# Kernel tuning notes

Hardware: AMD Instinct MI355X
Metric: run time of the kernel (lower is better)

Reference implementation:

```python
import jax, jax.numpy as jnp
import numpy as np

NUM_ITERATIONS = 3
NUM_SLOTS = 8
SLOT_SIZE = 256
MLP_HIDDEN = 512
EPSILON = 1e-8
LN_EPS = 1e-5


def _ln(x, w, b):
    m = jnp.mean(x, axis=-1, keepdims=True)
    v = jnp.var(x, axis=-1, keepdims=True)
    return (x - m) * jax.lax.rsqrt(v + LN_EPS) * w + b


def _gru_cell(x, h, w_ih, w_hh, b_ih, b_hh):
    # torch.nn.GRUCell semantics; gates ordered [r, z, n]
    gi = x @ w_ih.T + b_ih
    gh = h @ w_hh.T + b_hh
    ir, iz, inn = jnp.split(gi, 3, axis=-1)
    hr, hz, hn = jnp.split(gh, 3, axis=-1)
    r = jax.nn.sigmoid(ir + hr)
    z = jax.nn.sigmoid(iz + hz)
    n = jnp.tanh(inn + r * hn)
    return (1.0 - z) * n + z * h


def setup_inputs() -> dict:
    key = jax.random.key(0)
    ks = jax.random.split(key, 12)
    D, H = SLOT_SIZE, MLP_HIDDEN
    s = 0.02
    return {
        "inputs": jax.random.normal(ks[0], (64, 4096, D), dtype=jnp.float32),
        "noise": jax.random.normal(ks[1], (64, NUM_SLOTS, D), dtype=jnp.float32),
        "ln_in_w": jnp.ones((D,), jnp.float32), "ln_in_b": jnp.zeros((D,), jnp.float32),
        "ln_slots_w": jnp.ones((D,), jnp.float32), "ln_slots_b": jnp.zeros((D,), jnp.float32),
        "ln_mlp_w": jnp.ones((D,), jnp.float32), "ln_mlp_b": jnp.zeros((D,), jnp.float32),
        "slots_mu": jax.random.normal(ks[2], (1, 1, D), jnp.float32) * s,
        "slots_log_sigma": jnp.zeros((1, 1, D), jnp.float32),
        "Wq": jax.random.normal(ks[3], (D, D), jnp.float32) * s,
        "Wk": jax.random.normal(ks[4], (D, D), jnp.float32) * s,
        "Wv": jax.random.normal(ks[5], (D, D), jnp.float32) * s,
        "gru_w_ih": jax.random.normal(ks[6], (3 * D, D), jnp.float32) * s,
        "gru_w_hh": jax.random.normal(ks[7], (3 * D, D), jnp.float32) * s,
        "gru_b_ih": jnp.zeros((3 * D,), jnp.float32),
        "gru_b_hh": jnp.zeros((3 * D,), jnp.float32),
        "mlp_w1": jax.random.normal(ks[8], (H, D), jnp.float32) * s,
        "mlp_b1": jnp.zeros((H,), jnp.float32),
        "mlp_w2": jax.random.normal(ks[9], (D, H), jnp.float32) * s,
        "mlp_b2": jnp.zeros((D,), jnp.float32),
    }


def reference(inputs, noise, ln_in_w, ln_in_b, ln_slots_w, ln_slots_b, ln_mlp_w, ln_mlp_b,
              slots_mu, slots_log_sigma, Wq, Wk, Wv,
              gru_w_ih, gru_w_hh, gru_b_ih, gru_b_hh,
              mlp_w1, mlp_b1, mlp_w2, mlp_b2):
    B, N, D = inputs.shape
    S = NUM_SLOTS
    x = _ln(inputs, ln_in_w, ln_in_b)            # [B,N,D]
    k = x @ Wk.T                                  # [B,N,D]
    v = x @ Wv.T                                  # [B,N,D]
    slots = slots_mu + jnp.exp(slots_log_sigma) * noise   # [B,S,D]
    scale = D ** (-0.5)
    for _ in range(NUM_ITERATIONS):
        slots_prev = slots
        s_n = _ln(slots, ln_slots_w, ln_slots_b)
        q = (s_n @ Wq.T) * scale                  # [B,S,D]
        attn_logits = jnp.einsum('bnd,bsd->bns', k, q)
        attn = jax.nn.softmax(attn_logits, axis=-1) + EPSILON
        attn = attn / jnp.sum(attn, axis=-2, keepdims=True)   # renorm over inputs
        updates = jnp.einsum('bns,bnd->bsd', attn, v)          # [B,S,D]
        slots = _gru_cell(updates.reshape(-1, D), slots_prev.reshape(-1, D),
                          gru_w_ih, gru_w_hh, gru_b_ih, gru_b_hh).reshape(B, S, D)
        h = jax.nn.relu(_ln(slots, ln_mlp_w, ln_mlp_b) @ mlp_w1.T + mlp_b1)
        slots = slots + (h @ mlp_w2.T + mlp_b2)
    return slots
```

## Files before the change

kernel.cpp:

```cpp
#include <hip/hip_runtime.h>

#define CB 64
#define CN 4096
#define CD 256
#define CS 8
#define CH 512

typedef __bf16 bf16_t;
typedef bf16_t bf16x8 __attribute__((ext_vector_type(8)));
typedef float f32x4 __attribute__((ext_vector_type(4)));

__device__ __forceinline__ unsigned short f2bf(float f){
  unsigned int u = __builtin_bit_cast(unsigned int, f);
  u += 0x7FFFu + ((u >> 16) & 1u);
  return (unsigned short)(u >> 16);
}

__device__ __forceinline__ f32x4 mfma16(bf16x8 a, bf16x8 b, f32x4 c){
  return __builtin_amdgcn_mfma_f32_16x16x32_bf16(a, b, c, 0, 0, 0);
}

__device__ __forceinline__ void gl_lds16(const void* g, void* l){
  __builtin_amdgcn_global_load_lds(
      (const __attribute__((address_space(1))) unsigned int*)g,
      (__attribute__((address_space(3))) unsigned int*)l, 16, 0, 0);
}

__global__ __launch_bounds__(256) void k_ln(const float* __restrict__ in,
    const float* __restrict__ gw, const float* __restrict__ gb,
    unsigned short* __restrict__ x){
  int blk = blockIdx.x;
  int b = blk >> 6, nt = blk & 63;
  int wv = threadIdx.x >> 6, l = threadIdx.x & 63;
  const float* base = in + ((size_t)b*CN + (size_t)nt*64) * CD;
  unsigned short* xb = x + ((size_t)b*CN + (size_t)nt*64) * CD;
  float4 w4 = *(const float4*)(gw + 4*l);
  float4 b4 = *(const float4*)(gb + 4*l);
  for(int i = 0; i < 16; i++){
    int r = wv*16 + i;
    float4 v = *(const float4*)(base + (size_t)r*CD + 4*l);
    float s1 = v.x + v.y + v.z + v.w;
    float s2 = v.x*v.x + v.y*v.y + v.z*v.z + v.w*v.w;
    #pragma unroll
    for(int m = 1; m < 64; m <<= 1){ s1 += __shfl_xor(s1, m); s2 += __shfl_xor(s2, m); }
    float mean = s1 * (1.0f/CD);
    float var  = fmaxf(s2 * (1.0f/CD) - mean*mean, 0.0f);
    float rstd = rsqrtf(var + 1e-5f);
    float y0 = (v.x - mean)*rstd*w4.x + b4.x;
    float y1 = (v.y - mean)*rstd*w4.y + b4.y;
    float y2 = (v.z - mean)*rstd*w4.z + b4.z;
    float y3 = (v.w - mean)*rstd*w4.w + b4.w;
    uint2 p;
    p.x = (unsigned)f2bf(y0) | ((unsigned)f2bf(y1) << 16);
    p.y = (unsigned)f2bf(y2) | ((unsigned)f2bf(y3) << 16);
    *(uint2*)(xb + (size_t)r*CD + 4*l) = p;
  }
}

__global__ __launch_bounds__(256) void k_setup(
    const float* __restrict__ Wq, const float* __restrict__ Wk,
    const float* __restrict__ wih, const float* __restrict__ Wv,
    const float* __restrict__ whh, const float* __restrict__ w1,
    const float* __restrict__ w2, const float* __restrict__ noise,
    const float* __restrict__ mu, const float* __restrict__ lsig,
    unsigned short* __restrict__ M1T, unsigned short* __restrict__ Mih_bf,
    unsigned short* __restrict__ Whh_bf, unsigned short* __restrict__ w1_bf,
    unsigned short* __restrict__ w2_bf, float* __restrict__ slots){
  int bid = blockIdx.x, tid = threadIdx.x;
  if(bid < 256){
    int ep = bid, e = tid;
    float acc = 0.0f;
    for(int d = 0; d < 256; d++) acc = fmaf(Wq[(size_t)d*256 + e], Wk[(size_t)d*256 + ep], acc);
    M1T[(size_t)ep*256 + e] = f2bf(acc * 0.0625f);
  } else if(bid < 1024){
    int j = bid - 256, e = tid;
    float acc = 0.0f;
    for(int d = 0; d < 256; d++) acc = fmaf(wih[(size_t)j*256 + d], Wv[(size_t)d*256 + e], acc);
    Mih_bf[(size_t)j*256 + e] = f2bf(acc);
  } else if(bid < 1792){
    int idx = (bid - 1024)*256 + tid;
    Whh_bf[idx] = f2bf(whh[idx]);
  } else if(bid < 2304){
    int idx = (bid - 1792)*256 + tid;
    w1_bf[idx] = f2bf(w1[idx]);
  } else if(bid < 2816){
    int idx = (bid - 2304)*256 + tid;
    w2_bf[idx] = f2bf(w2[idx]);
  } else {
    int idx = (bid - 2816)*256 + tid;
    int d = idx & 255;
    slots[idx] = mu[d] + __expf(lsig[d]) * noise[idx];
  }
}

__global__ __launch_bounds__(256) void k_qt(const float* __restrict__ slots,
    const float* __restrict__ lw, const float* __restrict__ lb,
    const unsigned short* __restrict__ M1T, unsigned short* __restrict__ qt,
    float* __restrict__ U, float* __restrict__ den){
  __shared__ unsigned short sn[16*264];
  int b = blockIdx.x;
  int tid = threadIdx.x;
  float4 z4 = {0.f, 0.f, 0.f, 0.f};
  float* Ub = U + (size_t)b*CS*CD;
  *(float4*)(Ub + tid*8)     = z4;
  *(float4*)(Ub + tid*8 + 4) = z4;
  if(tid < CS) den[b*CS + tid] = 0.0f;

  int wv = tid >> 6, l = tid & 63;
  int lm = l & 15, lg = l >> 4;
  float4 w4 = *(const float4*)(lw + 4*l);
  float4 b4 = *(const float4*)(lb + 4*l);
  for(int i = 0; i < 2; i++){
    int r = wv*2 + i;
    float4 v = *(const float4*)(slots + ((size_t)b*CS + r)*CD + 4*l);
    float s1 = v.x + v.y + v.z + v.w;
    float s2 = v.x*v.x + v.y*v.y + v.z*v.z + v.w*v.w;
    #pragma unroll
    for(int m = 1; m < 64; m <<= 1){ s1 += __shfl_xor(s1, m); s2 += __shfl_xor(s2, m); }
    float mean = s1 * (1.0f/CD);
    float var  = fmaxf(s2 * (1.0f/CD) - mean*mean, 0.0f);
    float rstd = rsqrtf(var + 1e-5f);
    float y0 = (v.x - mean)*rstd*w4.x + b4.x;
    float y1 = (v.y - mean)*rstd*w4.y + b4.y;
    float y2 = (v.z - mean)*rstd*w4.z + b4.z;
    float y3 = (v.w - mean)*rstd*w4.w + b4.w;
    uint2 p;
    p.x = (unsigned)f2bf(y0) | ((unsigned)f2bf(y1) << 16);
    p.y = (unsigned)f2bf(y2) | ((unsigned)f2bf(y3) << 16);
    *(uint2*)(&sn[r*264 + 4*l]) = p;
    uint2 zz; zz.x = 0u; zz.y = 0u;
    *(uint2*)(&sn[(r+8)*264 + 4*l]) = zz;
  }
  __syncthreads();
  bf16x8 af[8];
  #pragma unroll
  for(int k = 0; k < 8; k++) af[k] = *(const bf16x8*)(&sn[lm*264 + k*32 + lg*8]);
  #pragma unroll
  for(int ntile = 0; ntile < 4; ntile++){
    int ep = wv*64 + ntile*16 + lm;
    f32x4 acc = {0.f, 0.f, 0.f, 0.f};
    const unsigned short* mrow = M1T + (size_t)ep*CD;
    #pragma unroll
    for(int k = 0; k < 8; k++){
      bf16x8 bf = *(const bf16x8*)(mrow + k*32 + lg*8);
      acc = mfma16(af[k], bf, acc);
    }
    #pragma unroll
    for(int reg = 0; reg < 4; reg++){
      int s = lg*4 + reg;
      qt[((size_t)b*16 + s)*CD + ep] = f2bf(acc[reg]);
    }
  }
}

__global__ __launch_bounds__(256) void k_attn(const unsigned short* __restrict__ x,
    const unsigned short* __restrict__ qt, float* __restrict__ U, float* __restrict__ den){
  __shared__ unsigned short xt[64*256];
  __shared__ unsigned short pt[16*72];
  int b = blockIdx.x >> 4, chunk = blockIdx.x & 15;
  int wv = threadIdx.x >> 6, l = threadIdx.x & 63;
  int lm = l & 15, lg = l >> 4;

  bf16x8 qb[8];
  const unsigned short* qrow = qt + ((size_t)b*16 + lm)*CD;
  #pragma unroll
  for(int k = 0; k < 8; k++) qb[k] = *(const bf16x8*)(qrow + k*32 + lg*8);

  f32x4 uacc[4];
  #pragma unroll
  for(int nt = 0; nt < 4; nt++){ f32x4 z = {0.f,0.f,0.f,0.f}; uacc[nt] = z; }
  float dacc = 0.0f;

  const unsigned short* xbatch = x + (size_t)b*CN*CD + (size_t)chunk*256*CD;

  for(int t = 0; t < 4; t++){
    const unsigned short* xtile = xbatch + (size_t)t*64*CD;
    __syncthreads();
    #pragma unroll
    for(int k2 = 0; k2 < 8; k2++){
      int r0 = wv*16 + k2*2;
      int row = r0 + (l >> 5);
      int c = l & 31;
      int f = (row ^ (row >> 3)) & 7;
      const unsigned short* g = xtile + (size_t)row*CD + (size_t)(c ^ f)*8;
      gl_lds16(g, &xt[r0*CD]);
    }
    __syncthreads();

    f32x4 c4 = {0.f, 0.f, 0.f, 0.f};
    int rowl = wv*16 + lm;
    int f1 = (rowl ^ (rowl >> 3)) & 7;
    #pragma unroll
    for(int k = 0; k < 8; k++){
      int cc = (k*4 + lg) ^ f1;
      bf16x8 a = *(const bf16x8*)(&xt[rowl*256 + cc*8]);
      c4 = mfma16(a, qb[k], c4);
    }
    float pv[4];
    #pragma unroll
    for(int reg = 0; reg < 4; reg++){
      float v = (lm < 8) ? c4[reg] : -1e30f;
      float mx = v;
      #pragma unroll
      for(int m = 1; m < 16; m <<= 1) mx = fmaxf(mx, __shfl_xor(mx, m));
      float e = __expf(v - mx);
      float s = e;
      #pragma unroll
      for(int m = 1; m < 16; m <<= 1) s += __shfl_xor(s, m);
      float p = (lm < 8) ? (e/s + 1e-8f) : 0.0f;
      dacc += p;
      pv[reg] = p;
    }
    int rbase = wv*16 + lg*4;
    unsigned int p01 = (unsigned)f2bf(pv[0]) | ((unsigned)f2bf(pv[1]) << 16);
    unsigned int p23 = (unsigned)f2bf(pv[2]) | ((unsigned)f2bf(pv[3]) << 16);
    *(unsigned int*)(&pt[lm*72 + rbase])     = p01;
    *(unsigned int*)(&pt[lm*72 + rbase + 2]) = p23;
    __syncthreads();

    #pragma unroll
    for(int ks = 0; ks < 2; ks++){
      bf16x8 a = *(const bf16x8*)(&pt[lm*72 + ks*32 + lg*8]);
      int rb = ks*32 + lg*8;
      #pragma unroll
      for(int nt = 0; nt < 4; nt++){
        int e = wv*64 + nt*16 + lm;
        bf16x8 bfr;
        #pragma unroll
        for(int j = 0; j < 8; j++){
          int row2 = rb + j;
          int f2 = (row2 ^ (row2 >> 3)) & 7;
          int cidx = (e >> 3) ^ f2;
          unsigned short tv = xt[row2*256 + cidx*8 + (e & 7)];
          bfr[j] = __builtin_bit_cast(bf16_t, tv);
        }
        uacc[nt] = mfma16(a, bfr, uacc[nt]);
      }
    }
  }

  dacc += __shfl_xor(dacc, 16);
  dacc += __shfl_xor(dacc, 32);
  if(l < 8) atomicAdd(&den[b*CS + l], dacc);
  if(lg < 2){
    #pragma unroll
    for(int nt = 0; nt < 4; nt++){
      #pragma unroll
      for(int reg = 0; reg < 4; reg++){
        int s = lg*4 + reg;
        atomicAdd(&U[((size_t)b*CS + s)*CD + wv*64 + nt*16 + lm], uacc[nt][reg]);
      }
    }
  }
}

__global__ __launch_bounds__(512) void k_update(
    const float* __restrict__ U, const float* slots,
    const float* __restrict__ den,
    const unsigned short* __restrict__ Mih, const unsigned short* __restrict__ Whh,
    const unsigned short* __restrict__ w1b, const unsigned short* __restrict__ w2b,
    const float* __restrict__ bih, const float* __restrict__ bhh,
    const float* __restrict__ lmw, const float* __restrict__ lmb,
    const float* __restrict__ b1, const float* __restrict__ b2,
    float* out){
  __shared__ unsigned short A1[16*264];
  __shared__ unsigned short SBf[16*264];
  __shared__ unsigned short A3[16*520];
  __shared__ float G1[8*777];
  __shared__ float G2[8*777];
  __shared__ float Hh[8*257];
  int b = blockIdx.x, tid = threadIdx.x;
  int l = tid & 63, lm = l & 15, lg = l >> 4;
  int wv = tid >> 6;

  for(int i = tid; i < 8*264; i += 512){ A1[8*264 + i] = 0; SBf[8*264 + i] = 0; }
  for(int i = tid; i < 8*520; i += 512) A3[8*520 + i] = 0;
  {
    int t2 = tid & 255;
    int r = t2 >> 5, c = (t2 & 31)*8;
    const float* src = ((tid < 256) ? U : slots) + ((size_t)b*CS + r)*CD + c;
    float4 a0 = *(const float4*)src, a1 = *(const float4*)(src + 4);
    uint4 pk;
    pk.x = (unsigned)f2bf(a0.x) | ((unsigned)f2bf(a0.y) << 16);
    pk.y = (unsigned)f2bf(a0.z) | ((unsigned)f2bf(a0.w) << 16);
    pk.z = (unsigned)f2bf(a1.x) | ((unsigned)f2bf(a1.y) << 16);
    pk.w = (unsigned)f2bf(a1.z) | ((unsigned)f2bf(a1.w) << 16);
    if(tid < 256) *(uint4*)(&A1[r*264 + c]) = pk;
    else          *(uint4*)(&SBf[r*264 + c]) = pk;
  }
  __syncthreads();

  {
    const unsigned short* W = (wv < 4) ? Mih : Whh;
    const unsigned short* As = (wv < 4) ? A1 : SBf;
    float* G = (wv < 4) ? G1 : G2;
    int w4 = wv & 3;
    bf16x8 af[8];
    #pragma unroll
    for(int k = 0; k < 8; k++) af[k] = *(const bf16x8*)(&As[lm*264 + k*32 + lg*8]);
    const unsigned short* brow = W + ((size_t)(w4*192 + lm))*CD + lg*8;
    bf16x8 bv[8], bw[8];
    #pragma unroll
    for(int k = 0; k < 8; k++) bv[k] = *(const bf16x8*)(brow + k*32);
    for(int t = 0; t < 12; t++){
      if(t < 11){
        const unsigned short* bn = brow + (size_t)(t + 1)*16*CD;
        #pragma unroll
        for(int k = 0; k < 8; k++) bw[k] = *(const bf16x8*)(bn + k*32);
      }
      f32x4 acc = {0.f,0.f,0.f,0.f};
      #pragma unroll
      for(int k = 0; k < 8; k++) acc = mfma16(af[k], bv[k], acc);
      if(lg < 2){
        int cb = w4*192 + t*16 + lm;
        #pragma unroll
        for(int reg = 0; reg < 4; reg++) G[(lg*4 + reg)*777 + cb] = acc[reg];
      }
      #pragma unroll
      for(int k = 0; k < 8; k++) bv[k] = bw[k];
    }
  }
  __syncthreads();

  {
    int r = wv;
    float invd = 1.0f / den[b*CS + r];
    const float* srow = slots + ((size_t)b*CS + r)*CD;
    float hv[4]; float s1 = 0.f, s2 = 0.f;
    #pragma unroll
    for(int i = 0; i < 4; i++){
      int c = l + 64*i;
      float gr = G1[r*777 + c]*invd + bih[c] + G2[r*777 + c] + bhh[c];
      float gz = G1[r*777 + 256 + c]*invd + bih[256 + c] + G2[r*777 + 256 + c] + bhh[256 + c];
      float gn = G1[r*777 + 512 + c]*invd + bih[512 + c];
      float hn = G2[r*777 + 512 + c] + bhh[512 + c];
      float rr = 1.0f/(1.0f + __expf(-gr));
      float zz = 1.0f/(1.0f + __expf(-gz));
      float nn = tanhf(gn + rr*hn);
      float h = (1.0f - zz)*nn + zz*srow[c];
      hv[i] = h; Hh[r*257 + c] = h; s1 += h; s2 += h*h;
    }
    #pragma unroll
    for(int m = 1; m < 64; m <<= 1){ s1 += __shfl_xor(s1, m); s2 += __shfl_xor(s2, m); }
    float mean = s1 * (1.0f/CD);
    float var  = fmaxf(s2 * (1.0f/CD) - mean*mean, 0.0f);
    float rstd = rsqrtf(var + 1e-5f);
    #pragma unroll
    for(int i = 0; i < 4; i++){
      int c = l + 64*i;
      A1[r*264 + c] = f2bf((hv[i] - mean)*rstd*lmw[c] + lmb[c]);
    }
  }
  __syncthreads();

  {
    bf16x8 af[8];
    #pragma unroll
    for(int k = 0; k < 8; k++) af[k] = *(const bf16x8*)(&A1[lm*264 + k*32 + lg*8]);
    const unsigned short* brow = w1b + ((size_t)(wv*64 + lm))*CD + lg*8;
    for(int t = 0; t < 4; t++){
      const unsigned short* bn = brow + (size_t)t*16*CD;
      f32x4 acc = {0.f,0.f,0.f,0.f};
      #pragma unroll
      for(int k = 0; k < 8; k++){
        bf16x8 bv = *(const bf16x8*)(bn + k*32);
        acc = mfma16(af[k], bv, acc);
      }
      if(lg < 2){
        int c = wv*64 + t*16 + lm;
        float bb = b1[c];
        #pragma unroll
        for(int reg = 0; reg < 4; reg++)
          A3[(lg*4 + reg)*520 + c] = f2bf(fmaxf(acc[reg] + bb, 0.0f));
      }
    }
  }
  __syncthreads();

  {
    bf16x8 af[16];
    #pragma unroll
    for(int k = 0; k < 16; k++) af[k] = *(const bf16x8*)(&A3[lm*520 + k*32 + lg*8]);
    const unsigned short* brow = w2b + ((size_t)(wv*32 + lm))*CH + lg*8;
    for(int t = 0; t < 2; t++){
      const unsigned short* bn = brow + (size_t)t*16*CH;
      f32x4 acc = {0.f,0.f,0.f,0.f};
      #pragma unroll
      for(int k = 0; k < 16; k++){
        bf16x8 bv = *(const bf16x8*)(bn + k*32);
        acc = mfma16(af[k], bv, acc);
      }
      if(lg < 2){
        int c = wv*32 + t*16 + lm;
        float bb = b2[c];
        #pragma unroll
        for(int reg = 0; reg < 4; reg++){
          int row = lg*4 + reg;
          out[((size_t)b*CS + row)*CD + c] = acc[reg] + bb + Hh[row*257 + c];
        }
      }
    }
  }
}

extern "C" void kernel_launch(void* const* d_in, const int* in_sizes, int n_in,
                              void* d_out, int out_size, void* d_ws, size_t ws_size,
                              hipStream_t stream){
  const float* inputs = (const float*)d_in[0];
  const float* noise  = (const float*)d_in[1];
  const float* ln_in_w = (const float*)d_in[2];
  const float* ln_in_b = (const float*)d_in[3];
  const float* ln_sl_w = (const float*)d_in[4];
  const float* ln_sl_b = (const float*)d_in[5];
  const float* ln_ml_w = (const float*)d_in[6];
  const float* ln_ml_b = (const float*)d_in[7];
  const float* mu   = (const float*)d_in[8];
  const float* lsig = (const float*)d_in[9];
  const float* Wq  = (const float*)d_in[10];
  const float* Wk  = (const float*)d_in[11];
  const float* Wv  = (const float*)d_in[12];
  const float* wih = (const float*)d_in[13];
  const float* whh = (const float*)d_in[14];
  const float* bih = (const float*)d_in[15];
  const float* bhh = (const float*)d_in[16];
  const float* w1  = (const float*)d_in[17];
  const float* b1  = (const float*)d_in[18];
  const float* w2  = (const float*)d_in[19];
  const float* b2  = (const float*)d_in[20];

  char* ws = (char*)d_ws;
  size_t off = 0;
  unsigned short* x = (unsigned short*)(ws + off); off += (size_t)CB*CN*CD*2;
  float* slots = (float*)(ws + off); off += (size_t)CB*CS*CD*4;
  float* U     = (float*)(ws + off); off += (size_t)CB*CS*CD*4;
  float* den   = (float*)(ws + off); off += (size_t)CB*CS*4;
  unsigned short* qt     = (unsigned short*)(ws + off); off += (size_t)CB*16*CD*2;
  unsigned short* M1T    = (unsigned short*)(ws + off); off += (size_t)CD*CD*2;
  unsigned short* Mih_bf = (unsigned short*)(ws + off); off += (size_t)768*CD*2;
  unsigned short* Whh_bf = (unsigned short*)(ws + off); off += (size_t)768*CD*2;
  unsigned short* w1_bf  = (unsigned short*)(ws + off); off += (size_t)CH*CD*2;
  unsigned short* w2_bf  = (unsigned short*)(ws + off); off += (size_t)CD*CH*2;

  k_ln<<<4096, 256, 0, stream>>>(inputs, ln_in_w, ln_in_b, x);
  k_setup<<<3328, 256, 0, stream>>>(Wq, Wk, wih, Wv, whh, w1, w2, noise, mu, lsig,
                                    M1T, Mih_bf, Whh_bf, w1_bf, w2_bf, slots);

  for(int it = 0; it < 3; it++){
    k_qt<<<64, 256, 0, stream>>>(slots, ln_sl_w, ln_sl_b, M1T, qt, U, den);
    k_attn<<<1024, 256, 0, stream>>>(x, qt, U, den);
    float* dst = (it == 2) ? (float*)d_out : slots;
    k_update<<<64, 512, 0, stream>>>(U, slots, den,
        Mih_bf, Whh_bf, w1_bf, w2_bf,
        bih, bhh, ln_ml_w, ln_ml_b, b1, b2, dst);
  }
}
```

Measured before the change: 684.4 us.

## Fuse query projection into attention kernel and replace atomics with partial sums

Slot layernorm plus query projection now run inside each attention block, using shared memory aliased over the x tile, so the separate k_qt launch is removed once per iteration. Each of the 16 chunks per batch writes its own partial U and denominator, and k_update sums them, instead of float atomics into a zeroed buffer. This removes a launch and atomic contention. In exchange, each query projection is recomputed 16 times per batch, and k_update reads 16 partial buffers.

```diff
diff --git a/kernel.cpp b/kernel.cpp
--- a/kernel.cpp
+++ b/kernel.cpp
@@ -93,78 +93,67 @@
   }
 }
 
-__global__ __launch_bounds__(256) void k_qt(const float* __restrict__ slots,
-    const float* __restrict__ lw, const float* __restrict__ lb,
-    const unsigned short* __restrict__ M1T, unsigned short* __restrict__ qt,
-    float* __restrict__ U, float* __restrict__ den){
-  __shared__ unsigned short sn[16*264];
-  int b = blockIdx.x;
+__global__ __launch_bounds__(256) void k_attn(const unsigned short* __restrict__ x,
+    const float* __restrict__ slots, const float* __restrict__ lsw,
+    const float* __restrict__ lsb, const unsigned short* __restrict__ M1T,
+    float* __restrict__ Upart, float* __restrict__ dpart){
+  __shared__ unsigned short xt[64*256];
+  __shared__ unsigned short pt[16*72];
+  __shared__ float dred[4][8];
+  int b = blockIdx.x >> 4, chunk = blockIdx.x & 15;
   int tid = threadIdx.x;
-  float4 z4 = {0.f, 0.f, 0.f, 0.f};
-  float* Ub = U + (size_t)b*CS*CD;
-  *(float4*)(Ub + tid*8)     = z4;
-  *(float4*)(Ub + tid*8 + 4) = z4;
-  if(tid < CS) den[b*CS + tid] = 0.0f;
-
   int wv = tid >> 6, l = tid & 63;
   int lm = l & 15, lg = l >> 4;
-  float4 w4 = *(const float4*)(lw + 4*l);
-  float4 b4 = *(const float4*)(lb + 4*l);
-  for(int i = 0; i < 2; i++){
-    int r = wv*2 + i;
-    float4 v = *(const float4*)(slots + ((size_t)b*CS + r)*CD + 4*l);
-    float s1 = v.x + v.y + v.z + v.w;
-    float s2 = v.x*v.x + v.y*v.y + v.z*v.z + v.w*v.w;
-    #pragma unroll
-    for(int m = 1; m < 64; m <<= 1){ s1 += __shfl_xor(s1, m); s2 += __shfl_xor(s2, m); }
-    float mean = s1 * (1.0f/CD);
-    float var  = fmaxf(s2 * (1.0f/CD) - mean*mean, 0.0f);
-    float rstd = rsqrtf(var + 1e-5f);
-    float y0 = (v.x - mean)*rstd*w4.x + b4.x;
-    float y1 = (v.y - mean)*rstd*w4.y + b4.y;
-    float y2 = (v.z - mean)*rstd*w4.z + b4.z;
-    float y3 = (v.w - mean)*rstd*w4.w + b4.w;
-    uint2 p;
-    p.x = (unsigned)f2bf(y0) | ((unsigned)f2bf(y1) << 16);
-    p.y = (unsigned)f2bf(y2) | ((unsigned)f2bf(y3) << 16);
-    *(uint2*)(&sn[r*264 + 4*l]) = p;
-    uint2 zz; zz.x = 0u; zz.y = 0u;
-    *(uint2*)(&sn[(r+8)*264 + 4*l]) = zz;
-  }
-  __syncthreads();
-  bf16x8 af[8];
+
+  unsigned short* sn    = xt;
+  unsigned short* qtile = xt + 4224;
+  {
+    float4 w4 = *(const float4*)(lsw + 4*l);
+    float4 b4 = *(const float4*)(lsb + 4*l);
+    for(int i = 0; i < 2; i++){
+      int r = wv*2 + i;
+      float4 v = *(const float4*)(slots + ((size_t)b*CS + r)*CD + 4*l);
+      float s1 = v.x + v.y + v.z + v.w;
+      float s2 = v.x*v.x + v.y*v.y + v.z*v.z + v.w*v.w;
+      #pragma unroll
+      for(int m = 1; m < 64; m <<= 1){ s1 += __shfl_xor(s1, m); s2 += __shfl_xor(s2, m); }
+      float mean = s1 * (1.0f/CD);
+      float var  = fmaxf(s2 * (1.0f/CD) - mean*mean, 0.0f);
+      float rstd = rsqrtf(var + 1e-5f);
+      float y0 = (v.x - mean)*rstd*w4.x + b4.x;
+      float y1 = (v.y - mean)*rstd*w4.y + b4.y;
+      float y2 = (v.z - mean)*rstd*w4.z + b4.z;
+      float y3 = (v.w - mean)*rstd*w4.w + b4.w;
+      uint2 p;
+      p.x = (unsigned)f2bf(y0) | ((unsigned)f2bf(y1) << 16);
+      p.y = (unsigned)f2bf(y2) | ((unsigned)f2bf(y3) << 16);
+      *(uint2*)(&sn[r*264 + 4*l]) = p;
+      uint2 zz; zz.x = 0u; zz.y = 0u;
+      *(uint2*)(&sn[(r+8)*264 + 4*l]) = zz;
+    }
+    __syncthreads();
+    bf16x8 af[8];
+    #pragma unroll
+    for(int k = 0; k < 8; k++) af[k] = *(const bf16x8*)(&sn[lm*264 + k*32 + lg*8]);
+    #pragma unroll
+    for(int ntile = 0; ntile < 4; ntile++){
+      int ep = wv*64 + ntile*16 + lm;
+      f32x4 acc = {0.f, 0.f, 0.f, 0.f};
+      const unsigned short* mrow = M1T + (size_t)ep*CD;
+      #pragma unroll
+      for(int k = 0; k < 8; k++){
+        bf16x8 bf = *(const bf16x8*)(mrow + k*32 + lg*8);
+        acc = mfma16(af[k], bf, acc);
+      }
+      #pragma unroll
+      for(int reg = 0; reg < 4; reg++)
+        qtile[(lg*4 + reg)*264 + ep] = f2bf(acc[reg]);
+    }
+    __syncthreads();
+  }
+  bf16x8 qb[8];
   #pragma unroll
-  for(int k = 0; k < 8; k++) af[k] = *(const bf16x8*)(&sn[lm*264 + k*32 + lg*8]);
-  #pragma unroll
-  for(int ntile = 0; ntile < 4; ntile++){
-    int ep = wv*64 + ntile*16 + lm;
-    f32x4 acc = {0.f, 0.f, 0.f, 0.f};
-    const unsigned short* mrow = M1T + (size_t)ep*CD;
-    #pragma unroll
-    for(int k = 0; k < 8; k++){
-      bf16x8 bf = *(const bf16x8*)(mrow + k*32 + lg*8);
-      acc = mfma16(af[k], bf, acc);
-    }
-    #pragma unroll
-    for(int reg = 0; reg < 4; reg++){
-      int s = lg*4 + reg;
-      qt[((size_t)b*16 + s)*CD + ep] = f2bf(acc[reg]);
-    }
-  }
-}
-
-__global__ __launch_bounds__(256) void k_attn(const unsigned short* __restrict__ x,
-    const unsigned short* __restrict__ qt, float* __restrict__ U, float* __restrict__ den){
-  __shared__ unsigned short xt[64*256];
-  __shared__ unsigned short pt[16*72];
-  int b = blockIdx.x >> 4, chunk = blockIdx.x & 15;
-  int wv = threadIdx.x >> 6, l = threadIdx.x & 63;
-  int lm = l & 15, lg = l >> 4;
-
-  bf16x8 qb[8];
-  const unsigned short* qrow = qt + ((size_t)b*16 + lm)*CD;
-  #pragma unroll
-  for(int k = 0; k < 8; k++) qb[k] = *(const bf16x8*)(qrow + k*32 + lg*8);
+  for(int k = 0; k < 8; k++) qb[k] = *(const bf16x8*)(&qtile[lm*264 + k*32 + lg*8]);
 
   f32x4 uacc[4];
   #pragma unroll
@@ -241,22 +230,27 @@
 
   dacc += __shfl_xor(dacc, 16);
   dacc += __shfl_xor(dacc, 32);
-  if(l < 8) atomicAdd(&den[b*CS + l], dacc);
+  if(l < 8) dred[wv][l] = dacc;
   if(lg < 2){
+    float* Ub = Upart + (((size_t)chunk*CB + b)*CS)*CD;
     #pragma unroll
     for(int nt = 0; nt < 4; nt++){
       #pragma unroll
       for(int reg = 0; reg < 4; reg++){
         int s = lg*4 + reg;
-        atomicAdd(&U[((size_t)b*CS + s)*CD + wv*64 + nt*16 + lm], uacc[nt][reg]);
-      }
-    }
-  }
+        Ub[(size_t)s*CD + wv*64 + nt*16 + lm] = uacc[nt][reg];
+      }
+    }
+  }
+  __syncthreads();
+  if(tid < 8)
+    dpart[((size_t)chunk*CB + b)*CS + tid] =
+        dred[0][tid] + dred[1][tid] + dred[2][tid] + dred[3][tid];
 }
 
 __global__ __launch_bounds__(512) void k_update(
-    const float* __restrict__ U, const float* slots,
-    const float* __restrict__ den,
+    const float* __restrict__ Upart, const float* slots,
+    const float* __restrict__ dpart,
     const unsigned short* __restrict__ Mih, const unsigned short* __restrict__ Whh,
     const unsigned short* __restrict__ w1b, const unsigned short* __restrict__ w2b,
     const float* __restrict__ bih, const float* __restrict__ bhh,
@@ -275,18 +269,34 @@
 
   for(int i = tid; i < 8*264; i += 512){ A1[8*264 + i] = 0; SBf[8*264 + i] = 0; }
   for(int i = tid; i < 8*520; i += 512) A3[8*520 + i] = 0;
-  {
+  if(tid < 256){
+    int r = tid >> 5, c = (tid & 31)*8;
+    float s0=0.f,s1=0.f,s2=0.f,s3=0.f,s4=0.f,s5=0.f,s6=0.f,s7=0.f;
+    #pragma unroll
+    for(int ch = 0; ch < 16; ch++){
+      const float* Up = Upart + (((size_t)ch*CB + b)*CS + r)*CD + c;
+      float4 a0 = *(const float4*)Up;
+      float4 a1 = *(const float4*)(Up + 4);
+      s0 += a0.x; s1 += a0.y; s2 += a0.z; s3 += a0.w;
+      s4 += a1.x; s5 += a1.y; s6 += a1.z; s7 += a1.w;
+    }
+    uint4 pk;
+    pk.x = (unsigned)f2bf(s0) | ((unsigned)f2bf(s1) << 16);
+    pk.y = (unsigned)f2bf(s2) | ((unsigned)f2bf(s3) << 16);
+    pk.z = (unsigned)f2bf(s4) | ((unsigned)f2bf(s5) << 16);
+    pk.w = (unsigned)f2bf(s6) | ((unsigned)f2bf(s7) << 16);
+    *(uint4*)(&A1[r*264 + c]) = pk;
+  } else {
     int t2 = tid & 255;
     int r = t2 >> 5, c = (t2 & 31)*8;
-    const float* src = ((tid < 256) ? U : slots) + ((size_t)b*CS + r)*CD + c;
+    const float* src = slots + ((size_t)b*CS + r)*CD + c;
     float4 a0 = *(const float4*)src, a1 = *(const float4*)(src + 4);
     uint4 pk;
     pk.x = (unsigned)f2bf(a0.x) | ((unsigned)f2bf(a0.y) << 16);
     pk.y = (unsigned)f2bf(a0.z) | ((unsigned)f2bf(a0.w) << 16);
     pk.z = (unsigned)f2bf(a1.x) | ((unsigned)f2bf(a1.y) << 16);
     pk.w = (unsigned)f2bf(a1.z) | ((unsigned)f2bf(a1.w) << 16);
-    if(tid < 256) *(uint4*)(&A1[r*264 + c]) = pk;
-    else          *(uint4*)(&SBf[r*264 + c]) = pk;
+    *(uint4*)(&SBf[r*264 + c]) = pk;
   }
   __syncthreads();
 
@@ -324,7 +334,10 @@
 
   {
     int r = wv;
-    float invd = 1.0f / den[b*CS + r];
+    float dsum = dpart[((size_t)(l & 15)*CB + b)*CS + r];
+    #pragma unroll
+    for(int m = 1; m < 16; m <<= 1) dsum += __shfl_xor(dsum, m);
+    float invd = 1.0f / dsum;
     const float* srow = slots + ((size_t)b*CS + r)*CD;
     float hv[4]; float s1 = 0.f, s2 = 0.f;
     #pragma unroll
@@ -432,9 +445,8 @@
   size_t off = 0;
   unsigned short* x = (unsigned short*)(ws + off); off += (size_t)CB*CN*CD*2;
   float* slots = (float*)(ws + off); off += (size_t)CB*CS*CD*4;
-  float* U     = (float*)(ws + off); off += (size_t)CB*CS*CD*4;
-  float* den   = (float*)(ws + off); off += (size_t)CB*CS*4;
-  unsigned short* qt     = (unsigned short*)(ws + off); off += (size_t)CB*16*CD*2;
+  float* Upart = (float*)(ws + off); off += (size_t)16*CB*CS*CD*4;
+  float* dpart = (float*)(ws + off); off += (size_t)16*CB*CS*4;
   unsigned short* M1T    = (unsigned short*)(ws + off); off += (size_t)CD*CD*2;
   unsigned short* Mih_bf = (unsigned short*)(ws + off); off += (size_t)768*CD*2;
   unsigned short* Whh_bf = (unsigned short*)(ws + off); off += (size_t)768*CD*2;
@@ -446,10 +458,9 @@
                                     M1T, Mih_bf, Whh_bf, w1_bf, w2_bf, slots);
 
   for(int it = 0; it < 3; it++){
-    k_qt<<<64, 256, 0, stream>>>(slots, ln_sl_w, ln_sl_b, M1T, qt, U, den);
-    k_attn<<<1024, 256, 0, stream>>>(x, qt, U, den);
+    k_attn<<<1024, 256, 0, stream>>>(x, slots, ln_sl_w, ln_sl_b, M1T, Upart, dpart);
     float* dst = (it == 2) ? (float*)d_out : slots;
-    k_update<<<64, 512, 0, stream>>>(U, slots, den,
+    k_update<<<64, 512, 0, stream>>>(Upart, slots, dpart,
         Mih_bf, Whh_bf, w1_bf, w2_bf,
         bih, bhh, ln_ml_w, ln_ml_b, b1, b2, dst);
   }
```

Result: no change. 680.1 us (-0.6%).
